# Kernel optimization log

Hardware: AMD Instinct MI355X
Metric: run time of the kernel (lower is better)

Reference implementation:

```python
import jax, jax.numpy as jnp
import numpy as np

B, T, K = 1024, 1024, 48
START, STOP = 46, 47
NEG = -10000.0


def setup_inputs() -> dict:
    key = jax.random.key(0)
    k1, k2 = jax.random.split(key)
    feats = jax.random.normal(k1, (B, T, K), dtype=jnp.float32)
    transitions = jax.random.normal(k2, (K, K), dtype=jnp.float32)
    # CRF constraints exactly as in __init__: no transition into START, none out of STOP
    transitions = transitions.at[START, :].set(NEG).at[:, STOP].set(NEG)
    return {"feats": feats, "transitions": transitions}


def _viterbi_one(feats, transitions):
    # feats: [T, K]; transitions[next_tag, prev_tag]: [K, K]
    init = jnp.full((K,), NEG, dtype=feats.dtype).at[START].set(0.0)

    def step(forward_var, feat):
        # scores[next, prev] = forward_var[prev] + transitions[next, prev]
        scores = forward_var[None, :] + transitions
        bptr = jnp.argmax(scores, axis=1)                 # [K] best prev per next
        new_fv = jnp.max(scores, axis=1) + feat           # [K]
        return new_fv, bptr

    forward_var, bptrs = jax.lax.scan(step, init, feats)  # bptrs: [T, K]
    terminal = forward_var + transitions[STOP]
    best = jnp.argmax(terminal)
    path_score = terminal[best]

    # backtrack: carry = tag at time t, emit it, move to bptrs[t][tag]
    def back(tag, bp):
        return bp[tag], tag

    _, best_path = jax.lax.scan(back, best, bptrs, reverse=True)  # [T] in time order
    return path_score, best_path


def reference(feats, transitions):
    # vmap the (faithful, per-sequence) Viterbi decode over the batch
    scores, paths = jax.vmap(_viterbi_one, in_axes=(0, None))(feats, transitions)
    return scores, paths
```

## Files before the change

### kernel.cpp

```cpp
#include <hip/hip_runtime.h>
#include <float.h>


#define BB 1024
#define TT 1024
#define KK 48
#define CC 16
#define LL 64
#define NEGV -10000.0f

__device__ __forceinline__ float rdlane(float v, int l) {
  return __int_as_float(__builtin_amdgcn_readlane(__float_as_int(v), l));
}
__device__ __forceinline__ float max3f(float a, float b, float c) {
  return fmaxf(fmaxf(a, b), c);
}


#define FSTEP(T_, FEAT_)                                                   \
  {                                                                        \
    float fvr[KK];                                                         \
    _Pragma("unroll") for (int j = 0; j < 12; ++j) {                       \
      float4 v4 = *(const float4*)(&fvbuf[4 * j]);                         \
      fvr[4 * j + 0] = v4.x; fvr[4 * j + 1] = v4.y;                        \
      fvr[4 * j + 2] = v4.z; fvr[4 * j + 3] = v4.w;                        \
    }                                                                      \
    float s_[KK];                                                          \
    _Pragma("unroll") for (int p = 0; p < KK; ++p) {                       \
      s_[p] = fvr[p] + tr[p];                                              \
    }                                                                      \
    float part[16];                                                        \
    _Pragma("unroll") for (int g = 0; g < 16; ++g) {                       \
      part[g] = max3f(s_[3 * g], s_[3 * g + 1], s_[3 * g + 2]);            \
    }                                                                      \
    float q0 = max3f(part[0], part[1], part[2]);                           \
    float q1 = max3f(part[3], part[4], part[5]);                           \
    float q2 = max3f(part[6], part[7], part[8]);                           \
    float q3 = max3f(part[9], part[10], part[11]);                         \
    float q4 = max3f(part[12], part[13], part[14]);                        \
    float m_ = fmaxf(max3f(q0, q1, q2), max3f(q3, q4, part[15]));          \
    mp[(size_t)(T_)*KK] = m_;                                              \
    fv = m_ + (FEAT_);                                                     \
    __builtin_amdgcn_wave_barrier();                                       \
    fvbuf[lane] = fv;                                                      \
    __builtin_amdgcn_wave_barrier();                                       \
  }

__global__ __launch_bounds__(64, 1) void viterbi_fwd_mx(
    const float* __restrict__ feats, const float* __restrict__ trans,
    float* __restrict__ scores, float* __restrict__ mx,
    int* __restrict__ bestArr) {
  __shared__ __align__(16) float fvbuf[64];
  const int lane = threadIdx.x;
  const int b = blockIdx.x;
  const int rl = (lane < KK) ? lane : (KK - 1);

  float tr[KK];
#pragma unroll
  for (int j = 0; j < 12; ++j) {
    float4 t4 = *(const float4*)(trans + rl * KK + 4 * j);
    tr[4 * j + 0] = t4.x; tr[4 * j + 1] = t4.y;
    tr[4 * j + 2] = t4.z; tr[4 * j + 3] = t4.w;
  }
#pragma unroll
  for (int j = 0; j < KK; ++j) asm volatile("" : "+v"(tr[j]));
  const float tstop = trans[(KK - 1) * KK + rl];

  const float* fp = feats + (size_t)b * TT * KK + rl;
  float* mp = mx + (size_t)b * TT * KK + rl;

  float fv = (lane == 46) ? 0.0f : NEGV;
  fvbuf[lane] = fv;
  __builtin_amdgcn_wave_barrier();

  if (lane < KK) {
    float fA[8], fB[8];
#pragma unroll
    for (int k = 0; k < 8; ++k) fA[k] = fp[(size_t)k * KK];

    for (int t0 = 0; t0 < TT; t0 += 16) {
#pragma unroll
      for (int k = 0; k < 8; ++k)
        fB[k] = fp[(size_t)((t0 + 8 + k) & (TT - 1)) * KK];
#pragma unroll
      for (int u = 0; u < 8; ++u) FSTEP(t0 + u, fA[u]);
#pragma unroll
      for (int k = 0; k < 8; ++k)
        fA[k] = fp[(size_t)((t0 + 16 + k) & (TT - 1)) * KK];
#pragma unroll
      for (int u = 0; u < 8; ++u) FSTEP(t0 + 8 + u, fB[u]);
    }
  }

  float v = (lane < KK) ? (fv + tstop) : -FLT_MAX;
  int idx = lane;
#pragma unroll
  for (int off = 32; off >= 1; off >>= 1) {
    float ov = __shfl_xor(v, off);
    int oi = __shfl_xor(idx, off);
    bool take = (ov > v) || (ov == v && oi < idx);
    v = take ? ov : v;
    idx = take ? oi : idx;
  }
  if (lane == 0) { scores[b] = v; bestArr[b] = idx; }
}

__global__ __launch_bounds__(64, 1) void viterbi_bwd_mx(
    const float* __restrict__ feats, const float* __restrict__ trans,
    const float* __restrict__ mx, const int* __restrict__ bestArr,
    float* __restrict__ path) {
  __shared__ float tl[KK * KK];
  const int lane = threadIdx.x;
  const int b = blockIdx.x;
  const int rl = (lane < KK) ? lane : (KK - 1);
  for (int i = lane; i < KK * KK; i += 64) tl[i] = trans[i];
  __syncthreads();

  const float* fp = feats + (size_t)b * TT * KK + rl;
  const float* mp = mx + (size_t)b * TT * KK + rl;
  int tag = bestArr[b];

  float topA = mp[(size_t)(TT - 1) * KK];
  float MA[8], FE[8], MB[8], FB2[8];
#pragma unroll
  for (int u = 0; u < 8; ++u) {
    MA[u] = mp[(size_t)(TT - 2 - u) * KK];
    FE[u] = fp[(size_t)(TT - 2 - u) * KK];
  }

  int myv = 0;
  for (int jb = TT - 1; jb >= 15; jb -= 16) {
#pragma unroll
    for (int u = 0; u < 8; ++u) {
      int r = jb - 9 - u; int rc = r < 0 ? 0 : r;
      MB[u] = mp[(size_t)rc * KK];
      FB2[u] = fp[(size_t)rc * KK];
    }
#pragma unroll
    for (int u = 0; u < 8; ++u) {
      const int j = jb - u;
      if (lane == (j & 63)) myv = tag;
      if ((j & 63) == 0) path[(size_t)b * TT + j + lane] = (float)myv;
      float Tg = (u == 0) ? topA : MA[u - 1];
      float target = rdlane(Tg, tag);
      float s = (MA[u] + FE[u]) + tl[tag * KK + rl];
      unsigned long long bal = __ballot(s == target);
      tag = (int)__builtin_ctzll(bal);
    }
    float topB = MA[7];
#pragma unroll
    for (int u = 0; u < 8; ++u) {
      int r = jb - 17 - u; int rc = r < 0 ? 0 : r;
      MA[u] = mp[(size_t)rc * KK];
      FE[u] = fp[(size_t)rc * KK];
    }
#pragma unroll
    for (int u = 0; u < 8; ++u) {
      const int j = jb - 8 - u;
      if (lane == (j & 63)) myv = tag;
      if ((j & 63) == 0) path[(size_t)b * TT + j + lane] = (float)myv;
      float Tg = (u == 0) ? topB : MB[u - 1];
      float target = rdlane(Tg, tag);
      float s = (MB[u] + FB2[u]) + tl[tag * KK + rl];
      unsigned long long bal = __ballot(s == target);
      tag = (int)__builtin_ctzll(bal);
    }
    topA = MB[7];
  }
}


__global__ __launch_bounds__(64, 1) void viterbi_fwd_f(
    const float* __restrict__ feats, const float* __restrict__ trans,
    float* __restrict__ scores, unsigned char* __restrict__ bptr,
    int* __restrict__ bestArr) {
  __shared__ __align__(16) float fvbuf[64];
  const int lane = threadIdx.x;
  const int b = blockIdx.x;
  const int rl = (lane < KK) ? lane : (KK - 1);

  float tr[KK];
#pragma unroll
  for (int j = 0; j < 12; ++j) {
    float4 t4 = *(const float4*)(trans + rl * KK + 4 * j);
    tr[4 * j + 0] = t4.x; tr[4 * j + 1] = t4.y;
    tr[4 * j + 2] = t4.z; tr[4 * j + 3] = t4.w;
  }
  const float tstop = trans[(KK - 1) * KK + rl];

  if (lane < KK) fvbuf[lane] = (lane == 46) ? 0.0f : NEGV;
  __builtin_amdgcn_wave_barrier();

  const float* fp = feats + (size_t)b * TT * KK + rl;
  unsigned char* bp = bptr + (size_t)b * TT * KK + lane;

  float fbuf[4];
#pragma unroll
  for (int k = 0; k < 4; ++k) fbuf[k] = fp[(size_t)k * KK];

  float fv = NEGV;
  for (int t0 = 0; t0 < TT; t0 += 4) {
#pragma unroll
    for (int u = 0; u < 4; ++u) {
      const int t = t0 + u;
      float fvr[KK];
#pragma unroll
      for (int j = 0; j < 12; ++j) {
        float4 v4 = *(const float4*)(&fvbuf[4 * j]);
        fvr[4 * j + 0] = v4.x; fvr[4 * j + 1] = v4.y;
        fvr[4 * j + 2] = v4.z; fvr[4 * j + 3] = v4.w;
      }
      __builtin_amdgcn_wave_barrier();

      float bs0 = fvr[0] + tr[0], bs1 = fvr[12] + tr[12];
      float bs2 = fvr[24] + tr[24], bs3 = fvr[36] + tr[36];
      int bi0 = 0, bi1 = 12, bi2 = 24, bi3 = 36;
#pragma unroll
      for (int p = 1; p < 12; ++p) {
        float s0 = fvr[p] + tr[p];
        float s1 = fvr[12 + p] + tr[12 + p];
        float s2 = fvr[24 + p] + tr[24 + p];
        float s3 = fvr[36 + p] + tr[36 + p];
        if (s0 > bs0) { bs0 = s0; bi0 = p; }
        if (s1 > bs1) { bs1 = s1; bi1 = 12 + p; }
        if (s2 > bs2) { bs2 = s2; bi2 = 24 + p; }
        if (s3 > bs3) { bs3 = s3; bi3 = 36 + p; }
      }
      bool c1 = bs1 > bs0;
      float m01 = c1 ? bs1 : bs0; int i01 = c1 ? bi1 : bi0;
      bool c3 = bs3 > bs2;
      float m23 = c3 ? bs3 : bs2; int i23 = c3 ? bi3 : bi2;
      bool cf = m23 > m01;
      float m = cf ? m23 : m01; int bpi = cf ? i23 : i01;

      float nfv = m + fbuf[u];
      int tpre = t + 4; if (tpre >= TT) tpre = 0;
      fbuf[u] = fp[(size_t)tpre * KK];

      if (lane < KK) {
        bp[(size_t)t * KK] = (unsigned char)bpi;
        fvbuf[lane] = nfv;
        fv = nfv;
      }
      __builtin_amdgcn_wave_barrier();
    }
  }

  float v = (lane < KK) ? (fv + tstop) : -FLT_MAX;
  int idx = lane;
#pragma unroll
  for (int off = 32; off >= 1; off >>= 1) {
    float ov = __shfl_xor(v, off);
    int oi = __shfl_xor(idx, off);
    bool take = (ov > v) || (ov == v && oi < idx);
    v = take ? ov : v;
    idx = take ? oi : idx;
  }
  if (lane == 0) { scores[b] = v; bestArr[b] = idx; }
}

__global__ __launch_bounds__(256) void bwd_map(
    const unsigned char* __restrict__ bptr, unsigned char* __restrict__ cmap) {
  const int lane = threadIdx.x & 63;
  const int wg = blockIdx.x * 4 + (threadIdx.x >> 6);
  const int b = wg >> 4;
  const int c = wg & (CC - 1);
  const int rl = (lane < KK) ? lane : (KK - 1);
  const unsigned char* bp = bptr + ((size_t)b * TT + (size_t)c * LL) * KK + rl;

  int x = rl;
  const int CH = 16;
  int cur[CH], nxt[CH];
#pragma unroll
  for (int j = 0; j < CH; ++j) cur[j] = bp[(size_t)(LL - CH + j) * KK];
  for (int tb = LL - CH; tb >= 0; tb -= CH) {
    if (tb >= CH) {
#pragma unroll
      for (int j = 0; j < CH; ++j) nxt[j] = bp[(size_t)(tb - CH + j) * KK];
    }
#pragma unroll
    for (int j = CH - 1; j >= 0; --j) x = __shfl(cur[j], x);
    if (tb >= CH) {
#pragma unroll
      for (int j = 0; j < CH; ++j) cur[j] = nxt[j];
    }
  }
  if (lane < KK) cmap[(size_t)wg * KK + lane] = (unsigned char)x;
}

__global__ __launch_bounds__(256) void bwd_entry(
    const unsigned char* __restrict__ cmap, const int* __restrict__ bestArr,
    int* __restrict__ entry) {
  const int lane = threadIdx.x & 63;
  const int b = blockIdx.x * 4 + (threadIdx.x >> 6);
  const int rl = (lane < KK) ? lane : (KK - 1);

  int rows[CC];
#pragma unroll
  for (int c = 0; c < CC; ++c) rows[c] = cmap[((size_t)b * CC + c) * KK + rl];

  int tag = bestArr[b];
  int ev = 0;
#pragma unroll
  for (int c = CC - 1; c >= 0; --c) {
    if (lane == c) ev = tag;
    tag = __shfl(rows[c], tag);
  }
  if (lane < CC) entry[b * CC + lane] = ev;
}

__global__ __launch_bounds__(256) void bwd_emit(
    const unsigned char* __restrict__ bptr, const int* __restrict__ entry,
    float* __restrict__ path) {
  const int lane = threadIdx.x & 63;
  const int wg = blockIdx.x * 4 + (threadIdx.x >> 6);
  const int b = wg >> 4;
  const int c = wg & (CC - 1);
  const int rl = (lane < KK) ? lane : (KK - 1);
  const unsigned char* bp = bptr + ((size_t)b * TT + (size_t)c * LL) * KK + rl;

  int x = entry[b * CC + c];
  int myv = 0;
  const int CH = 16;
  int cur[CH], nxt[CH];
#pragma unroll
  for (int j = 0; j < CH; ++j) cur[j] = bp[(size_t)(LL - CH + j) * KK];
  for (int tb = LL - CH; tb >= 0; tb -= CH) {
    if (tb >= CH) {
#pragma unroll
      for (int j = 0; j < CH; ++j) nxt[j] = bp[(size_t)(tb - CH + j) * KK];
    }
#pragma unroll
    for (int j = CH - 1; j >= 0; --j) {
      if (lane == tb + j) myv = x;
      x = __shfl(cur[j], x);
    }
    if (tb >= CH) {
#pragma unroll
      for (int j = 0; j < CH; ++j) cur[j] = nxt[j];
    }
  }
  path[(size_t)b * TT + (size_t)c * LL + lane] = (float)myv;
}

extern "C" void kernel_launch(void* const* d_in, const int* in_sizes, int n_in,
                              void* d_out, int out_size, void* d_ws,
                              size_t ws_size, hipStream_t stream) {
  const float* feats = (const float*)d_in[0];
  const float* trans = (const float*)d_in[1];
  float* out = (float*)d_out;

  const size_t MX_BYTES = (size_t)BB * TT * KK * sizeof(float);
  if (ws_size >= MX_BYTES + 4096) {
    float* mx = (float*)d_ws;
    int* bestArr = (int*)((char*)d_ws + MX_BYTES);
    viterbi_fwd_mx<<<dim3(BB), dim3(64), 0, stream>>>(feats, trans, out, mx,
                                                      bestArr);
    viterbi_bwd_mx<<<dim3(BB), dim3(64), 0, stream>>>(feats, trans, mx,
                                                      bestArr, out + BB);
  } else {
    unsigned char* bptr = (unsigned char*)d_ws;
    char* p = (char*)d_ws + (size_t)BB * TT * KK;
    int* bestArr = (int*)p;
    p += BB * sizeof(int);
    unsigned char* cmap = (unsigned char*)p;
    p += (size_t)BB * CC * KK;
    int* entry = (int*)p;

    viterbi_fwd_f<<<dim3(BB), dim3(64), 0, stream>>>(feats, trans, out, bptr,
                                                     bestArr);
    bwd_map<<<dim3(BB * CC / 4), dim3(256), 0, stream>>>(bptr, cmap);
    bwd_entry<<<dim3(BB / 4), dim3(256), 0, stream>>>(cmap, bestArr, entry);
    bwd_emit<<<dim3(BB * CC / 4), dim3(256), 0, stream>>>(bptr, entry,
                                                          out + BB);
  }
}
```

Measured before the change: 490.0 us.

## Prefer byte-backpointer Viterbi path with double-buffered feature prefetch over max-matrix path

The launcher now takes the uint8 backpointer pipeline (forward plus chunked map/entry/emit backtrack) whenever the workspace holds it, and uses the float max-matrix recompute path only as a fallback. Storing one byte per tag per step instead of a float cuts forward-pass write traffic and avoids recomputing comparisons during backtrack. The forward kernel is also reworked: features are prefetched in two 8-step register banks, the work is restricted to the 48 active lanes, and transition registers are pinned with empty asm. The cost is three extra small kernel launches and more register pressure in the forward kernel.

Result: slower. 818.3 us (+67.0%).

```diff
diff --git a/kernel.cpp b/kernel.cpp
--- a/kernel.cpp
+++ b/kernel.cpp
@@ -14,6 +14,185 @@
 }
 __device__ __forceinline__ float max3f(float a, float b, float c) {
   return fmaxf(fmaxf(a, b), c);
+}
+
+
+#define BSTEP(T_, FEAT_)                                                   \
+  {                                                                        \
+    float fvr[KK];                                                         \
+    _Pragma("unroll") for (int j = 0; j < 12; ++j) {                       \
+      float4 v4 = *(const float4*)(&fvbuf[4 * j]);                         \
+      fvr[4 * j + 0] = v4.x; fvr[4 * j + 1] = v4.y;                        \
+      fvr[4 * j + 2] = v4.z; fvr[4 * j + 3] = v4.w;                        \
+    }                                                                      \
+    float bs0 = fvr[0] + tr[0], bs1 = fvr[12] + tr[12];                    \
+    float bs2 = fvr[24] + tr[24], bs3 = fvr[36] + tr[36];                  \
+    int bi0 = 0, bi1 = 12, bi2 = 24, bi3 = 36;                             \
+    _Pragma("unroll") for (int p = 1; p < 12; ++p) {                       \
+      float s0 = fvr[p] + tr[p];                                           \
+      float s1 = fvr[12 + p] + tr[12 + p];                                 \
+      float s2 = fvr[24 + p] + tr[24 + p];                                 \
+      float s3 = fvr[36 + p] + tr[36 + p];                                 \
+      if (s0 > bs0) { bs0 = s0; bi0 = p; }                                 \
+      if (s1 > bs1) { bs1 = s1; bi1 = 12 + p; }                            \
+      if (s2 > bs2) { bs2 = s2; bi2 = 24 + p; }                            \
+      if (s3 > bs3) { bs3 = s3; bi3 = 36 + p; }                            \
+    }                                                                      \
+    bool c1 = bs1 > bs0;                                                   \
+    float m01 = c1 ? bs1 : bs0; int i01 = c1 ? bi1 : bi0;                  \
+    bool c3 = bs3 > bs2;                                                   \
+    float m23 = c3 ? bs3 : bs2; int i23 = c3 ? bi3 : bi2;                  \
+    bool cf = m23 > m01;                                                   \
+    float m = cf ? m23 : m01; int bpi = cf ? i23 : i01;                    \
+    bp[(size_t)(T_)*KK] = (unsigned char)bpi;                              \
+    fv = m + (FEAT_);                                                      \
+    __builtin_amdgcn_wave_barrier();                                       \
+    fvbuf[lane] = fv;                                                      \
+    __builtin_amdgcn_wave_barrier();                                       \
+  }
+
+__global__ __launch_bounds__(64, 1) void viterbi_fwd_bp(
+    const float* __restrict__ feats, const float* __restrict__ trans,
+    float* __restrict__ scores, unsigned char* __restrict__ bptr,
+    int* __restrict__ bestArr) {
+  __shared__ __align__(16) float fvbuf[64];
+  const int lane = threadIdx.x;
+  const int b = blockIdx.x;
+  const int rl = (lane < KK) ? lane : (KK - 1);
+
+  float tr[KK];
+#pragma unroll
+  for (int j = 0; j < 12; ++j) {
+    float4 t4 = *(const float4*)(trans + rl * KK + 4 * j);
+    tr[4 * j + 0] = t4.x; tr[4 * j + 1] = t4.y;
+    tr[4 * j + 2] = t4.z; tr[4 * j + 3] = t4.w;
+  }
+#pragma unroll
+  for (int j = 0; j < KK; ++j) asm volatile("" : "+v"(tr[j]));
+  const float tstop = trans[(KK - 1) * KK + rl];
+
+  const float* fp = feats + (size_t)b * TT * KK + rl;
+  unsigned char* bp = bptr + (size_t)b * TT * KK + rl;
+
+  float fv = (lane == 46) ? 0.0f : NEGV;
+  fvbuf[lane] = fv;
+  __builtin_amdgcn_wave_barrier();
+
+  if (lane < KK) {
+    float fA[8], fB[8];
+#pragma unroll
+    for (int k = 0; k < 8; ++k) fA[k] = fp[(size_t)k * KK];
+
+    for (int t0 = 0; t0 < TT; t0 += 16) {
+#pragma unroll
+      for (int k = 0; k < 8; ++k)
+        fB[k] = fp[(size_t)((t0 + 8 + k) & (TT - 1)) * KK];
+#pragma unroll
+      for (int u = 0; u < 8; ++u) BSTEP(t0 + u, fA[u]);
+#pragma unroll
+      for (int k = 0; k < 8; ++k)
+        fA[k] = fp[(size_t)((t0 + 16 + k) & (TT - 1)) * KK];
+#pragma unroll
+      for (int u = 0; u < 8; ++u) BSTEP(t0 + 8 + u, fB[u]);
+    }
+  }
+
+  float v = (lane < KK) ? (fv + tstop) : -FLT_MAX;
+  int idx = lane;
+#pragma unroll
+  for (int off = 32; off >= 1; off >>= 1) {
+    float ov = __shfl_xor(v, off);
+    int oi = __shfl_xor(idx, off);
+    bool take = (ov > v) || (ov == v && oi < idx);
+    v = take ? ov : v;
+    idx = take ? oi : idx;
+  }
+  if (lane == 0) { scores[b] = v; bestArr[b] = idx; }
+}
+
+
+__global__ __launch_bounds__(256) void bwd_map(
+    const unsigned char* __restrict__ bptr, unsigned char* __restrict__ cmap) {
+  const int lane = threadIdx.x & 63;
+  const int wg = blockIdx.x * 4 + (threadIdx.x >> 6);
+  const int b = wg >> 4;
+  const int c = wg & (CC - 1);
+  const int rl = (lane < KK) ? lane : (KK - 1);
+  const unsigned char* bp = bptr + ((size_t)b * TT + (size_t)c * LL) * KK + rl;
+
+  int x = rl;
+  const int CH = 16;
+  int cur[CH], nxt[CH];
+#pragma unroll
+  for (int j = 0; j < CH; ++j) cur[j] = bp[(size_t)(LL - CH + j) * KK];
+  for (int tb = LL - CH; tb >= 0; tb -= CH) {
+    if (tb >= CH) {
+#pragma unroll
+      for (int j = 0; j < CH; ++j) nxt[j] = bp[(size_t)(tb - CH + j) * KK];
+    }
+#pragma unroll
+    for (int j = CH - 1; j >= 0; --j) x = __shfl(cur[j], x);
+    if (tb >= CH) {
+#pragma unroll
+      for (int j = 0; j < CH; ++j) cur[j] = nxt[j];
+    }
+  }
+  if (lane < KK) cmap[(size_t)wg * KK + lane] = (unsigned char)x;
+}
+
+__global__ __launch_bounds__(256) void bwd_entry(
+    const unsigned char* __restrict__ cmap, const int* __restrict__ bestArr,
+    int* __restrict__ entry) {
+  const int lane = threadIdx.x & 63;
+  const int b = blockIdx.x * 4 + (threadIdx.x >> 6);
+  const int rl = (lane < KK) ? lane : (KK - 1);
+
+  int rows[CC];
+#pragma unroll
+  for (int c = 0; c < CC; ++c) rows[c] = cmap[((size_t)b * CC + c) * KK + rl];
+
+  int tag = bestArr[b];
+  int ev = 0;
+#pragma unroll
+  for (int c = CC - 1; c >= 0; --c) {
+    if (lane == c) ev = tag;
+    tag = __shfl(rows[c], tag);
+  }
+  if (lane < CC) entry[b * CC + lane] = ev;
+}
+
+__global__ __launch_bounds__(256) void bwd_emit(
+    const unsigned char* __restrict__ bptr, const int* __restrict__ entry,
+    float* __restrict__ path) {
+  const int lane = threadIdx.x & 63;
+  const int wg = blockIdx.x * 4 + (threadIdx.x >> 6);
+  const int b = wg >> 4;
+  const int c = wg & (CC - 1);
+  const int rl = (lane < KK) ? lane : (KK - 1);
+  const unsigned char* bp = bptr + ((size_t)b * TT + (size_t)c * LL) * KK + rl;
+
+  int x = entry[b * CC + c];
+  int myv = 0;
+  const int CH = 16;
+  int cur[CH], nxt[CH];
+#pragma unroll
+  for (int j = 0; j < CH; ++j) cur[j] = bp[(size_t)(LL - CH + j) * KK];
+  for (int tb = LL - CH; tb >= 0; tb -= CH) {
+    if (tb >= CH) {
+#pragma unroll
+      for (int j = 0; j < CH; ++j) nxt[j] = bp[(size_t)(tb - CH + j) * KK];
+    }
+#pragma unroll
+    for (int j = CH - 1; j >= 0; --j) {
+      if (lane == tb + j) myv = x;
+      x = __shfl(cur[j], x);
+    }
+    if (tb >= CH) {
+#pragma unroll
+      for (int j = 0; j < CH; ++j) cur[j] = nxt[j];
+    }
+  }
+  path[(size_t)b * TT + (size_t)c * LL + lane] = (float)myv;
 }
 
 
@@ -169,180 +348,6 @@
   }
 }
 
-
-__global__ __launch_bounds__(64, 1) void viterbi_fwd_f(
-    const float* __restrict__ feats, const float* __restrict__ trans,
-    float* __restrict__ scores, unsigned char* __restrict__ bptr,
-    int* __restrict__ bestArr) {
-  __shared__ __align__(16) float fvbuf[64];
-  const int lane = threadIdx.x;
-  const int b = blockIdx.x;
-  const int rl = (lane < KK) ? lane : (KK - 1);
-
-  float tr[KK];
-#pragma unroll
-  for (int j = 0; j < 12; ++j) {
-    float4 t4 = *(const float4*)(trans + rl * KK + 4 * j);
-    tr[4 * j + 0] = t4.x; tr[4 * j + 1] = t4.y;
-    tr[4 * j + 2] = t4.z; tr[4 * j + 3] = t4.w;
-  }
-  const float tstop = trans[(KK - 1) * KK + rl];
-
-  if (lane < KK) fvbuf[lane] = (lane == 46) ? 0.0f : NEGV;
-  __builtin_amdgcn_wave_barrier();
-
-  const float* fp = feats + (size_t)b * TT * KK + rl;
-  unsigned char* bp = bptr + (size_t)b * TT * KK + lane;
-
-  float fbuf[4];
-#pragma unroll
-  for (int k = 0; k < 4; ++k) fbuf[k] = fp[(size_t)k * KK];
-
-  float fv = NEGV;
-  for (int t0 = 0; t0 < TT; t0 += 4) {
-#pragma unroll
-    for (int u = 0; u < 4; ++u) {
-      const int t = t0 + u;
-      float fvr[KK];
-#pragma unroll
-      for (int j = 0; j < 12; ++j) {
-        float4 v4 = *(const float4*)(&fvbuf[4 * j]);
-        fvr[4 * j + 0] = v4.x; fvr[4 * j + 1] = v4.y;
-        fvr[4 * j + 2] = v4.z; fvr[4 * j + 3] = v4.w;
-      }
-      __builtin_amdgcn_wave_barrier();
-
-      float bs0 = fvr[0] + tr[0], bs1 = fvr[12] + tr[12];
-      float bs2 = fvr[24] + tr[24], bs3 = fvr[36] + tr[36];
-      int bi0 = 0, bi1 = 12, bi2 = 24, bi3 = 36;
-#pragma unroll
-      for (int p = 1; p < 12; ++p) {
-        float s0 = fvr[p] + tr[p];
-        float s1 = fvr[12 + p] + tr[12 + p];
-        float s2 = fvr[24 + p] + tr[24 + p];
-        float s3 = fvr[36 + p] + tr[36 + p];
-        if (s0 > bs0) { bs0 = s0; bi0 = p; }
-        if (s1 > bs1) { bs1 = s1; bi1 = 12 + p; }
-        if (s2 > bs2) { bs2 = s2; bi2 = 24 + p; }
-        if (s3 > bs3) { bs3 = s3; bi3 = 36 + p; }
-      }
-      bool c1 = bs1 > bs0;
-      float m01 = c1 ? bs1 : bs0; int i01 = c1 ? bi1 : bi0;
-      bool c3 = bs3 > bs2;
-      float m23 = c3 ? bs3 : bs2; int i23 = c3 ? bi3 : bi2;
-      bool cf = m23 > m01;
-      float m = cf ? m23 : m01; int bpi = cf ? i23 : i01;
-
-      float nfv = m + fbuf[u];
-      int tpre = t + 4; if (tpre >= TT) tpre = 0;
-      fbuf[u] = fp[(size_t)tpre * KK];
-
-      if (lane < KK) {
-        bp[(size_t)t * KK] = (unsigned char)bpi;
-        fvbuf[lane] = nfv;
-        fv = nfv;
-      }
-      __builtin_amdgcn_wave_barrier();
-    }
-  }
-
-  float v = (lane < KK) ? (fv + tstop) : -FLT_MAX;
-  int idx = lane;
-#pragma unroll
-  for (int off = 32; off >= 1; off >>= 1) {
-    float ov = __shfl_xor(v, off);
-    int oi = __shfl_xor(idx, off);
-    bool take = (ov > v) || (ov == v && oi < idx);
-    v = take ? ov : v;
-    idx = take ? oi : idx;
-  }
-  if (lane == 0) { scores[b] = v; bestArr[b] = idx; }
-}
-
-__global__ __launch_bounds__(256) void bwd_map(
-    const unsigned char* __restrict__ bptr, unsigned char* __restrict__ cmap) {
-  const int lane = threadIdx.x & 63;
-  const int wg = blockIdx.x * 4 + (threadIdx.x >> 6);
-  const int b = wg >> 4;
-  const int c = wg & (CC - 1);
-  const int rl = (lane < KK) ? lane : (KK - 1);
-  const unsigned char* bp = bptr + ((size_t)b * TT + (size_t)c * LL) * KK + rl;
-
-  int x = rl;
-  const int CH = 16;
-  int cur[CH], nxt[CH];
-#pragma unroll
-  for (int j = 0; j < CH; ++j) cur[j] = bp[(size_t)(LL - CH + j) * KK];
-  for (int tb = LL - CH; tb >= 0; tb -= CH) {
-    if (tb >= CH) {
-#pragma unroll
-      for (int j = 0; j < CH; ++j) nxt[j] = bp[(size_t)(tb - CH + j) * KK];
-    }
-#pragma unroll
-    for (int j = CH - 1; j >= 0; --j) x = __shfl(cur[j], x);
-    if (tb >= CH) {
-#pragma unroll
-      for (int j = 0; j < CH; ++j) cur[j] = nxt[j];
-    }
-  }
-  if (lane < KK) cmap[(size_t)wg * KK + lane] = (unsigned char)x;
-}
-
-__global__ __launch_bounds__(256) void bwd_entry(
-    const unsigned char* __restrict__ cmap, const int* __restrict__ bestArr,
-    int* __restrict__ entry) {
-  const int lane = threadIdx.x & 63;
-  const int b = blockIdx.x * 4 + (threadIdx.x >> 6);
-  const int rl = (lane < KK) ? lane : (KK - 1);
-
-  int rows[CC];
-#pragma unroll
-  for (int c = 0; c < CC; ++c) rows[c] = cmap[((size_t)b * CC + c) * KK + rl];
-
-  int tag = bestArr[b];
-  int ev = 0;
-#pragma unroll
-  for (int c = CC - 1; c >= 0; --c) {
-    if (lane == c) ev = tag;
-    tag = __shfl(rows[c], tag);
-  }
-  if (lane < CC) entry[b * CC + lane] = ev;
-}
-
-__global__ __launch_bounds__(256) void bwd_emit(
-    const unsigned char* __restrict__ bptr, const int* __restrict__ entry,
-    float* __restrict__ path) {
-  const int lane = threadIdx.x & 63;
-  const int wg = blockIdx.x * 4 + (threadIdx.x >> 6);
-  const int b = wg >> 4;
-  const int c = wg & (CC - 1);
-  const int rl = (lane < KK) ? lane : (KK - 1);
-  const unsigned char* bp = bptr + ((size_t)b * TT + (size_t)c * LL) * KK + rl;
-
-  int x = entry[b * CC + c];
-  int myv = 0;
-  const int CH = 16;
-  int cur[CH], nxt[CH];
-#pragma unroll
-  for (int j = 0; j < CH; ++j) cur[j] = bp[(size_t)(LL - CH + j) * KK];
-  for (int tb = LL - CH; tb >= 0; tb -= CH) {
-    if (tb >= CH) {
-#pragma unroll
-      for (int j = 0; j < CH; ++j) nxt[j] = bp[(size_t)(tb - CH + j) * KK];
-    }
-#pragma unroll
-    for (int j = CH - 1; j >= 0; --j) {
-      if (lane == tb + j) myv = x;
-      x = __shfl(cur[j], x);
-    }
-    if (tb >= CH) {
-#pragma unroll
-      for (int j = 0; j < CH; ++j) cur[j] = nxt[j];
-    }
-  }
-  path[(size_t)b * TT + (size_t)c * LL + lane] = (float)myv;
-}
-
 extern "C" void kernel_launch(void* const* d_in, const int* in_sizes, int n_in,
                               void* d_out, int out_size, void* d_ws,
                               size_t ws_size, hipStream_t stream) {
@@ -350,28 +355,34 @@
   const float* trans = (const float*)d_in[1];
   float* out = (float*)d_out;
 
-  const size_t MX_BYTES = (size_t)BB * TT * KK * sizeof(float);
-  if (ws_size >= MX_BYTES + 4096) {
+  const size_t BP_BYTES = (size_t)BB * TT * KK;
+  const size_t BEST_BYTES = (size_t)BB * sizeof(int);
+  const size_t CMAP_BYTES = (size_t)BB * CC * KK;
+  const size_t ENTRY_BYTES = (size_t)BB * CC * sizeof(int);
+  const size_t NEED = BP_BYTES + BEST_BYTES + CMAP_BYTES + ENTRY_BYTES;
+
+  if (ws_size >= NEED) {
+    unsigned char* bptr = (unsigned char*)d_ws;
+    char* p = (char*)d_ws + BP_BYTES;
+    int* bestArr = (int*)p;
+    p += BEST_BYTES;
+    unsigned char* cmap = (unsigned char*)p;
+    p += CMAP_BYTES;
+    int* entry = (int*)p;
+
+    viterbi_fwd_bp<<<dim3(BB), dim3(64), 0, stream>>>(feats, trans, out, bptr,
+                                                      bestArr);
+    bwd_map<<<dim3(BB * CC / 4), dim3(256), 0, stream>>>(bptr, cmap);
+    bwd_entry<<<dim3(BB / 4), dim3(256), 0, stream>>>(cmap, bestArr, entry);
+    bwd_emit<<<dim3(BB * CC / 4), dim3(256), 0, stream>>>(bptr, entry,
+                                                          out + BB);
+  } else {
+    const size_t MX_BYTES = (size_t)BB * TT * KK * sizeof(float);
     float* mx = (float*)d_ws;
     int* bestArr = (int*)((char*)d_ws + MX_BYTES);
     viterbi_fwd_mx<<<dim3(BB), dim3(64), 0, stream>>>(feats, trans, out, mx,
                                                       bestArr);
     viterbi_bwd_mx<<<dim3(BB), dim3(64), 0, stream>>>(feats, trans, mx,
                                                       bestArr, out + BB);
-  } else {
-    unsigned char* bptr = (unsigned char*)d_ws;
-    char* p = (char*)d_ws + (size_t)BB * TT * KK;
-    int* bestArr = (int*)p;
-    p += BB * sizeof(int);
-    unsigned char* cmap = (unsigned char*)p;
-    p += (size_t)BB * CC * KK;
-    int* entry = (int*)p;
-
-    viterbi_fwd_f<<<dim3(BB), dim3(64), 0, stream>>>(feats, trans, out, bptr,
-                                                     bestArr);
-    bwd_map<<<dim3(BB * CC / 4), dim3(256), 0, stream>>>(bptr, cmap);
-    bwd_entry<<<dim3(BB / 4), dim3(256), 0, stream>>>(cmap, bestArr, entry);
-    bwd_emit<<<dim3(BB * CC / 4), dim3(256), 0, stream>>>(bptr, entry,
-                                                          out + BB);
-  }
-}
+  }
+}
```
